# Kernel optimization log

Hardware: AMD Instinct MI355X
Metric: run time of the kernel (lower is better)

## Reference

```python
import jax, jax.numpy as jnp
import numpy as np

N0, N1, N2 = 100000, 25000, 6250
E0, E1, E2 = 600000, 150000, 37500
K = 6


def cheb_conv(x, edge_index, W, b):
    """torch_geometric ChebConv with sym normalization, lambda_max=2:
    L_hat = -D^{-1/2} A D^{-1/2}; T0=x, T1=L_hat x, Tk=2 L_hat T_{k-1} - T_{k-2}."""
    n = x.shape[0]
    src, dst = edge_index[0], edge_index[1]
    deg = jax.ops.segment_sum(jnp.ones(src.shape[0], x.dtype), src, num_segments=n)
    dinv = jnp.where(deg > 0, jax.lax.rsqrt(jnp.maximum(deg, 1.0)), 0.0)
    w = -(dinv[src] * dinv[dst])  # [E]

    def prop(h):  # (L_hat h)_i = sum_{j->i} w_ij h_j
        return jax.ops.segment_sum(w[:, None] * h[src], dst, num_segments=n)

    Tx0 = x
    out = Tx0 @ W[0]
    Tx1 = prop(x)
    out = out + Tx1 @ W[1]
    for k in range(2, W.shape[0]):
        Tx2 = 2.0 * prop(Tx1) - Tx0
        out = out + Tx2 @ W[k]
        Tx0, Tx1 = Tx1, Tx2
    return out + b


def pool(x, rows, cols, vals, n_out):
    # sparse.mm(D, x): y[r] += v * x[c]
    return jax.ops.segment_sum(vals[:, None] * x[cols], rows, num_segments=n_out)


def setup_inputs() -> dict:
    key = jax.random.key(0)
    ks = jax.random.split(key, 16)
    inp = {}
    inp["x"] = jax.random.normal(ks[0], (N0, 3), jnp.float32)
    inp["edge_index0"] = jax.random.randint(ks[1], (2, E0), 0, N0, jnp.int32)
    inp["edge_index1"] = jax.random.randint(ks[2], (2, E1), 0, N1, jnp.int32)
    inp["edge_index2"] = jax.random.randint(ks[3], (2, E2), 0, N2, jnp.int32)
    s = 0.05
    inp["W0"] = jax.random.normal(ks[4], (K, 3, 128), jnp.float32) * s
    inp["b0"] = jax.random.normal(ks[5], (128,), jnp.float32) * s
    inp["W1"] = jax.random.normal(ks[6], (K, 128, 128), jnp.float32) * s
    inp["b1"] = jax.random.normal(ks[7], (128,), jnp.float32) * s
    inp["W2"] = jax.random.normal(ks[8], (K, 128, 256), jnp.float32) * s
    inp["b2"] = jax.random.normal(ks[9], (256,), jnp.float32) * s
    inp["D0_rows"] = jax.random.randint(ks[10], (100000,), 0, N1, jnp.int32)
    inp["D0_cols"] = jax.random.randint(ks[11], (100000,), 0, N0, jnp.int32)
    inp["D0_vals"] = jax.random.uniform(ks[12], (100000,), jnp.float32)
    inp["D1_rows"] = jax.random.randint(ks[13], (25000,), 0, N2, jnp.int32)
    inp["D1_cols"] = jax.random.randint(ks[14], (25000,), 0, N1, jnp.int32)
    inp["D1_vals"] = jax.random.uniform(ks[15], (25000,), jnp.float32)
    k2 = jax.random.split(jax.random.fold_in(key, 1), 2)
    inp["linW"] = jax.random.normal(k2[0], (10, N2 * 256), jnp.float32) * 0.001
    inp["linb"] = jax.random.normal(k2[1], (10,), jnp.float32) * s
    return inp


def reference(x, edge_index0, edge_index1, edge_index2, W0, b0, W1, b1, W2, b2,
              D0_rows, D0_cols, D0_vals, D1_rows, D1_cols, D1_vals, linW, linb):
    h = jax.nn.relu(cheb_conv(x, edge_index0, W0, b0))      # [N0,128]
    h = pool(h, D0_rows, D0_cols, D0_vals, N1)               # [N1,128]
    h = jax.nn.relu(cheb_conv(h, edge_index1, W1, b1))      # [N1,128]
    h = pool(h, D1_rows, D1_cols, D1_vals, N2)               # [N2,128]
    h = cheb_conv(h, edge_index2, W2, b2)                    # [N2,256]
    Z = linW @ h.reshape(-1) + linb                           # [10]
    return Z
```

## Files before the change

kernel.cpp:

```cpp
#include <hip/hip_runtime.h>


namespace {
constexpr int cN0 = 100000, cN1 = 25000, cN2 = 6250;
constexpr int cE0 = 600000, cE1 = 150000, cE2 = 37500;
constexpr int cD  = cN2 * 256;

constexpr int JN[5]  = {cN0, cN1, cN2, cN1, cN2};
constexpr int JE[5]  = {cE0, cE1, cE2, 100000, 25000};
constexpr int JB[5]  = {391, 98, 25, 98, 25};
constexpr int JBBASE[6] = {0, 391, 489, 514, 612, 637};
constexpr int TB = 637;
constexpr int JCB[5] = {293, 74, 19, 49, 13};
constexpr int JCBASE[6] = {0, 293, 367, 386, 435, 448};
constexpr int TCB = 448;
constexpr int CHUNK = 2048;
constexpr int BSTRIDE = 400;

constexpr int EBASE[5]   = {0, 600000, 750000, 787500, 887500};
constexpr int E_TOTAL    = 912500;
constexpr int NBASE[5]   = {0, 100096, 125184, 131584, 156672};
constexpr int NPAD_TOTAL = 163072;
constexpr int DEGBASE[3] = {0, 100000, 125000};
constexpr int DEG_TOTAL  = 131250;
constexpr int WPREP_TOTAL = 768 * 128 + 768 * 256 + 128 * 32;
constexpr int PREP_ALL_TOTAL = WPREP_TOTAL + DEG_TOTAL + cN0 + 10;
}

typedef __attribute__((ext_vector_type(8))) short short8;
typedef __attribute__((ext_vector_type(4))) float floatx4;

__device__ inline ushort f2h(float f) {
  union { _Float16 h; ushort u; } v;
  v.h = (_Float16)f;
  return v.u;
}
__device__ inline float h2f(unsigned lo16) {
  union { ushort u; _Float16 h; } v;
  v.u = (ushort)lo16;
  return (float)v.h;
}

__device__ inline int job_of_cb(int cb) {
  int j = 0;
  while (cb >= JCBASE[j + 1]) ++j;
  return j;
}
__device__ inline int job_of_bucket(int g) {
  int j = 0;
  while (g >= JBBASE[j + 1]) ++j;
  return j;
}

__global__ __launch_bounds__(256) void c1_count_kernel(
    const int* __restrict__ k0, const int* __restrict__ k1, const int* __restrict__ k2,
    const int* __restrict__ k3, const int* __restrict__ k4,
    const int* __restrict__ s0, const int* __restrict__ s1, const int* __restrict__ s2,
    int* __restrict__ degcnt, int* __restrict__ cntCB) {
  __shared__ int cnt[BSTRIDE];
  int cb = blockIdx.x;
  int j = job_of_cb(cb);
  int lb = cb - JCBASE[j];
  const int* keys;
  const int* srck = nullptr;
  int dbase = 0;
  switch (j) {
    case 0: keys = k0; srck = s0; dbase = DEGBASE[0]; break;
    case 1: keys = k1; srck = s1; dbase = DEGBASE[1]; break;
    case 2: keys = k2; srck = s2; dbase = DEGBASE[2]; break;
    case 3: keys = k3; break;
    default: keys = k4; break;
  }
  int nB = JB[j];
  for (int b = threadIdx.x; b < nB; b += 256) cnt[b] = 0;
  __syncthreads();
  int e0 = lb * CHUNK;
  int e1 = min(e0 + CHUNK, JE[j]);
  for (int e = e0 + threadIdx.x; e < e1; e += 256) {
    atomicAdd(&cnt[keys[e] >> 8], 1);
    if (srck) atomicAdd(&degcnt[dbase + srck[e]], 1);
  }
  __syncthreads();
  for (int b = threadIdx.x; b < nB; b += 256)
    cntCB[cb * BSTRIDE + b] = cnt[b];
}

__global__ __launch_bounds__(256) void c2a_scan_kernel(int* __restrict__ cntCB,
                                                       int* __restrict__ bucketTot,
                                                       const int* __restrict__ degcnt,
                                                       float* __restrict__ dinv) {
  __shared__ int s[256];
  int g = blockIdx.x;
  int j = job_of_bucket(g);
  int b = g - JBBASE[j];
  int cb0 = JCBASE[j], nCB = JCB[j];
  int carry = 0;
  for (int c0 = 0; c0 < nCB; c0 += 256) {
    int i = c0 + threadIdx.x;
    int v = (i < nCB) ? cntCB[(cb0 + i) * BSTRIDE + b] : 0;
    s[threadIdx.x] = v;
    __syncthreads();
    for (int d = 1; d < 256; d <<= 1) {
      int t = (threadIdx.x >= d) ? s[threadIdx.x - d] : 0;
      __syncthreads();
      s[threadIdx.x] += t;
      __syncthreads();
    }
    if (i < nCB) cntCB[(cb0 + i) * BSTRIDE + b] = carry + s[threadIdx.x] - v;
    carry += s[255];
    __syncthreads();
  }
  if (threadIdx.x == 0) bucketTot[g] = carry;
  int idx = blockIdx.x * 256 + threadIdx.x;
  if (idx < DEG_TOTAL) {
    int c = degcnt[idx];
    dinv[idx] = (c > 0) ? rsqrtf((float)c) : 0.f;
  }
}

__global__ __launch_bounds__(256) void c2b_scan_kernel(const int* __restrict__ bucketTot,
                                                       int* __restrict__ bucketBase) {
  __shared__ int s[256];
  int j = blockIdx.x;
  int g0 = JBBASE[j], nB = JB[j];
  int carry = 0;
  for (int c0 = 0; c0 < nB; c0 += 256) {
    int i = c0 + threadIdx.x;
    int v = (i < nB) ? bucketTot[g0 + i] : 0;
    s[threadIdx.x] = v;
    __syncthreads();
    for (int d = 1; d < 256; d <<= 1) {
      int t = (threadIdx.x >= d) ? s[threadIdx.x - d] : 0;
      __syncthreads();
      s[threadIdx.x] += t;
      __syncthreads();
    }
    if (i < nB) bucketBase[g0 + i] = carry + s[threadIdx.x] - v;
    carry += s[255];
    __syncthreads();
  }
}

__global__ __launch_bounds__(256) void c3_dst_kernel(
    const int* __restrict__ d0, const int* __restrict__ s0,
    const int* __restrict__ d1, const int* __restrict__ s1,
    const int* __restrict__ d2, const int* __restrict__ s2,
    const int* __restrict__ p0r, const int* __restrict__ p0c, const float* __restrict__ p0v,
    const int* __restrict__ p1r, const int* __restrict__ p1c, const float* __restrict__ p1v,
    const float* __restrict__ dinv,
    const int* __restrict__ cntCB, const int* __restrict__ bucketBase,
    int2* __restrict__ scatPairs) {
  __shared__ int base[BSTRIDE];
  int cb = blockIdx.x;
  int j = job_of_cb(cb);
  int lb = cb - JCBASE[j];
  const int* dk; const int* sk; const float* vv = nullptr;
  switch (j) {
    case 0: dk = d0; sk = s0; break;
    case 1: dk = d1; sk = s1; break;
    case 2: dk = d2; sk = s2; break;
    case 3: dk = p0r; sk = p0c; vv = p0v; break;
    default: dk = p1r; sk = p1c; vv = p1v; break;
  }
  int nB = JB[j];
  for (int b = threadIdx.x; b < nB; b += 256)
    base[b] = EBASE[j] + bucketBase[JBBASE[j] + b] + cntCB[cb * BSTRIDE + b];
  __syncthreads();
  int e0 = lb * CHUNK;
  int e1 = min(e0 + CHUNK, JE[j]);
  for (int e = e0 + threadIdx.x; e < e1; e += 256) {
    int d = dk[e];
    int s = sk[e];
    float w;
    if (j < 3) w = -(dinv[DEGBASE[j] + s] * dinv[DEGBASE[j] + d]);
    else w = vv[e];
    int pos = atomicAdd(&base[d >> 8], 1);
    scatPairs[pos] = make_int2(((d & 255) << 17) | s, __float_as_int(w));
  }
}

__global__ __launch_bounds__(256) void dcsr_kernel(const int2* __restrict__ scatPairs,
                                                   const int* __restrict__ bucketTot,
                                                   const int* __restrict__ bucketBase,
                                                   int* __restrict__ off,
                                                   int2* __restrict__ csrPairs) {
  __shared__ int cnt[256];
  __shared__ int sArr[256];
  __shared__ int cur[256];
  int g = blockIdx.x;
  int j = job_of_bucket(g);
  int b = g - JBBASE[j];
  int relBase = bucketBase[g];
  int st = EBASE[j] + relBase;
  int en = st + bucketTot[g];
  cnt[threadIdx.x] = 0;
  __syncthreads();
  for (int idx = st + threadIdx.x; idx < en; idx += 256)
    atomicAdd(&cnt[scatPairs[idx].x >> 17], 1);
  __syncthreads();
  int v = cnt[threadIdx.x];
  sArr[threadIdx.x] = v;
  __syncthreads();
  for (int d = 1; d < 256; d <<= 1) {
    int t = (threadIdx.x >= d) ? sArr[threadIdx.x - d] : 0;
    __syncthreads();
    sArr[threadIdx.x] += t;
    __syncthreads();
  }
  int excl = sArr[threadIdx.x] - v;
  int node = b * 256 + threadIdx.x;
  if (node < JN[j]) off[NBASE[j] + node] = relBase + excl;
  if (threadIdx.x == 0 && b == JB[j] - 1) off[NBASE[j] + JN[j]] = JE[j];
  cur[threadIdx.x] = st + excl;
  __syncthreads();
  for (int idx = st + threadIdx.x; idx < en; idx += 256) {
    int2 p = scatPairs[idx];
    int dl = p.x >> 17;
    int s = p.x & 0x1FFFF;
    int pos = atomicAdd(&cur[dl], 1);
    csrPairs[pos] = make_int2(s, p.y);
  }
}

__global__ __launch_bounds__(256) void csr_prop128h_kernel(
    const int* __restrict__ off, const int2* __restrict__ pairs,
    const ushort* __restrict__ hh, float* __restrict__ y, ushort* __restrict__ yh,
    const float* __restrict__ prev, float scale, int N) {
  int r = blockIdx.x * 16 + (threadIdx.x >> 4);
  int l = threadIdx.x & 15;
  if (r >= N) return;
  int s = off[r], e = off[r + 1];
  const uint4* h4 = (const uint4*)hh;
  float a0 = 0.f, a1 = 0.f, a2 = 0.f, a3 = 0.f;
  float a4 = 0.f, a5 = 0.f, a6 = 0.f, a7 = 0.f;
  int j = s;
  for (; j + 4 <= e; j += 4) {
    int2 p0 = pairs[j], p1 = pairs[j + 1], p2 = pairs[j + 2], p3 = pairs[j + 3];
    uint4 v0 = h4[(size_t)p0.x * 16 + l];
    uint4 v1 = h4[(size_t)p1.x * 16 + l];
    uint4 v2 = h4[(size_t)p2.x * 16 + l];
    uint4 v3 = h4[(size_t)p3.x * 16 + l];
    float w0 = __int_as_float(p0.y), w1 = __int_as_float(p1.y);
    float w2 = __int_as_float(p2.y), w3 = __int_as_float(p3.y);
    a0 += w0 * h2f(v0.x & 0xFFFFu) + w1 * h2f(v1.x & 0xFFFFu)
        + w2 * h2f(v2.x & 0xFFFFu) + w3 * h2f(v3.x & 0xFFFFu);
    a1 += w0 * h2f(v0.x >> 16) + w1 * h2f(v1.x >> 16)
        + w2 * h2f(v2.x >> 16) + w3 * h2f(v3.x >> 16);
    a2 += w0 * h2f(v0.y & 0xFFFFu) + w1 * h2f(v1.y & 0xFFFFu)
        + w2 * h2f(v2.y & 0xFFFFu) + w3 * h2f(v3.y & 0xFFFFu);
    a3 += w0 * h2f(v0.y >> 16) + w1 * h2f(v1.y >> 16)
        + w2 * h2f(v2.y >> 16) + w3 * h2f(v3.y >> 16);
    a4 += w0 * h2f(v0.z & 0xFFFFu) + w1 * h2f(v1.z & 0xFFFFu)
        + w2 * h2f(v2.z & 0xFFFFu) + w3 * h2f(v3.z & 0xFFFFu);
    a5 += w0 * h2f(v0.z >> 16) + w1 * h2f(v1.z >> 16)
        + w2 * h2f(v2.z >> 16) + w3 * h2f(v3.z >> 16);
    a6 += w0 * h2f(v0.w & 0xFFFFu) + w1 * h2f(v1.w & 0xFFFFu)
        + w2 * h2f(v2.w & 0xFFFFu) + w3 * h2f(v3.w & 0xFFFFu);
    a7 += w0 * h2f(v0.w >> 16) + w1 * h2f(v1.w >> 16)
        + w2 * h2f(v2.w >> 16) + w3 * h2f(v3.w >> 16);
  }
  for (; j < e; ++j) {
    int2 p = pairs[j];
    uint4 v0 = h4[(size_t)p.x * 16 + l];
    float w = __int_as_float(p.y);
    a0 += w * h2f(v0.x & 0xFFFFu);
    a1 += w * h2f(v0.x >> 16);
    a2 += w * h2f(v0.y & 0xFFFFu);
    a3 += w * h2f(v0.y >> 16);
    a4 += w * h2f(v0.z & 0xFFFFu);
    a5 += w * h2f(v0.z >> 16);
    a6 += w * h2f(v0.w & 0xFFFFu);
    a7 += w * h2f(v0.w >> 16);
  }
  a0 *= scale; a1 *= scale; a2 *= scale; a3 *= scale;
  a4 *= scale; a5 *= scale; a6 *= scale; a7 *= scale;
  if (prev) {
    const float4* p4 = (const float4*)prev;
    float4 pa = p4[(size_t)r * 32 + 2 * l];
    float4 pb = p4[(size_t)r * 32 + 2 * l + 1];
    a0 -= pa.x; a1 -= pa.y; a2 -= pa.z; a3 -= pa.w;
    a4 -= pb.x; a5 -= pb.y; a6 -= pb.z; a7 -= pb.w;
  }
  if (y) {
    float4* y4 = (float4*)y;
    y4[(size_t)r * 32 + 2 * l]     = make_float4(a0, a1, a2, a3);
    y4[(size_t)r * 32 + 2 * l + 1] = make_float4(a4, a5, a6, a7);
  }
  uint4 sp;
  sp.x = f2h(a0) | ((unsigned)f2h(a1) << 16);
  sp.y = f2h(a2) | ((unsigned)f2h(a3) << 16);
  sp.z = f2h(a4) | ((unsigned)f2h(a5) << 16);
  sp.w = f2h(a6) | ((unsigned)f2h(a7) << 16);
  ((uint4*)yh)[(size_t)r * 16 + l] = sp;
}

__global__ __launch_bounds__(256) void csr_prop3_kernel(
    const int* __restrict__ off, const int2* __restrict__ pairs,
    const float4* __restrict__ h, float4* __restrict__ y,
    const float4* __restrict__ prev, float scale, int N,
    ushort* __restrict__ yh, int kout) {
  int t = blockIdx.x * 256 + threadIdx.x;
  int r = t >> 2;
  int q = t & 3;
  if (r >= N) return;
  int s = off[r], e = off[r + 1];
  float ax = 0.f, ay = 0.f, az = 0.f;
  for (int j = s + q; j < e; j += 4) {
    int2 p = pairs[j];
    float4 hv = h[p.x];
    float w = __int_as_float(p.y);
    ax += w * hv.x; ay += w * hv.y; az += w * hv.z;
  }
  ax += __shfl_xor(ax, 1); ay += __shfl_xor(ay, 1); az += __shfl_xor(az, 1);
  ax += __shfl_xor(ax, 2); ay += __shfl_xor(ay, 2); az += __shfl_xor(az, 2);
  if (q == 0) {
    float4 v = make_float4(scale * ax, scale * ay, scale * az, 0.f);
    if (prev) {
      float4 pv = prev[r];
      v.x -= pv.x; v.y -= pv.y; v.z -= pv.z;
    }
    y[r] = v;
    uint2 sp = make_uint2(f2h(v.x) | ((unsigned)f2h(v.y) << 16), (unsigned)f2h(v.z));
    *(uint2*)(yh + (size_t)r * 32 + kout * 4) = sp;
  }
}

__global__ __launch_bounds__(256, 2) void h0_mfma_kernel(
    const ushort* __restrict__ Ah, const ushort* __restrict__ W0h,
    const float* __restrict__ b0, ushort* __restrict__ h0h, int M) {
  __shared__ ushort Al[64][40];
  __shared__ ushort Bl[128][40];
  __shared__ ushort Hs[64][128];
  const int tid = threadIdx.x;
  const int rowBase = blockIdx.x * 64;
  const int wave = tid >> 6;
  const int lane = tid & 63;
  const int m16 = lane & 15;
  const int quad = lane >> 4;
  {
    int sRow = tid >> 2;
    int sK8 = (tid & 3) * 8;
    int row = rowBase + sRow;
    uint4 av = make_uint4(0, 0, 0, 0);
    if (row < M) av = *(const uint4*)(Ah + (size_t)row * 32 + sK8);
    *(uint4*)&Al[sRow][sK8] = av;
  }
#pragma unroll
  for (int l = 0; l < 2; ++l) {
    int lin = tid + l * 256;
    int bRow = lin >> 2;
    int bK8 = (lin & 3) * 8;
    *(uint4*)&Bl[bRow][bK8] = *(const uint4*)(W0h + (size_t)bRow * 32 + bK8);
  }
  __syncthreads();
  short8 a = *(const short8*)&Al[wave * 16 + m16][quad * 8];
  floatx4 acc[8];
#pragma unroll
  for (int c = 0; c < 8; ++c) {
    floatx4 z;
    z[0] = 0.f; z[1] = 0.f; z[2] = 0.f; z[3] = 0.f;
    short8 b = *(const short8*)&Bl[c * 16 + m16][quad * 8];
    acc[c] = __builtin_amdgcn_mfma_f32_16x16x32_f16(a, b, z, 0, 0, 0);
  }
#pragma unroll
  for (int c = 0; c < 8; ++c) {
    int col = c * 16 + m16;
    float bv = b0[col];
#pragma unroll
    for (int r = 0; r < 4; ++r)
      Hs[wave * 16 + quad * 4 + r][col] = f2h(fmaxf(acc[c][r] + bv, 0.f));
  }
  __syncthreads();
  const uint4* ls = (const uint4*)&Hs[0][0];
  uint4* gd = (uint4*)(h0h + (size_t)rowBase * 128);
#pragma unroll
  for (int i = 0; i < 4; ++i) {
    int idx = tid + i * 256;
    if (rowBase + (idx >> 4) < M) gd[idx] = ls[idx];
  }
}

__global__ void prep_all_kernel(const float* __restrict__ W0, const float* __restrict__ W1,
                                const float* __restrict__ W2, ushort* __restrict__ W0h,
                                ushort* __restrict__ Wt1, ushort* __restrict__ Wt2,
                                int* __restrict__ degcnt,
                                const float* __restrict__ x, float4* __restrict__ Tb,
                                ushort* __restrict__ Ah,
                                float* __restrict__ out, const float* __restrict__ linb) {
  int i = blockIdx.x * 256 + threadIdx.x;
  if (i < 768 * 128) {
    int k = i / 128, n = i - k * 128;
    Wt1[(size_t)n * 768 + k] = f2h(W1[i]);
  } else if (i < 768 * 128 + 768 * 256) {
    int i2 = i - 768 * 128;
    int k = i2 / 256, n = i2 - k * 256;
    Wt2[(size_t)n * 768 + k] = f2h(W2[i2]);
  } else if (i < WPREP_TOTAL) {
    int i3 = i - 768 * 128 - 768 * 256;
    int col = i3 >> 5, k = i3 & 31;
    int a = k >> 2, jj = k & 3;
    float v = (k < 24 && jj < 3) ? W0[(a * 3 + jj) * 128 + col] : 0.f;
    W0h[(size_t)col * 32 + k] = f2h(v);
  } else if (i < WPREP_TOTAL + DEG_TOTAL) {
    degcnt[i - WPREP_TOTAL] = 0;
  } else if (i < WPREP_TOTAL + DEG_TOTAL + cN0) {
    int r = i - (WPREP_TOTAL + DEG_TOTAL);
    float x0 = x[3 * r], x1 = x[3 * r + 1], x2 = x[3 * r + 2];
    Tb[r] = make_float4(x0, x1, x2, 0.f);
    uint4 z = make_uint4(0, 0, 0, 0);
    uint4 first = make_uint4(f2h(x0) | ((unsigned)f2h(x1) << 16), (unsigned)f2h(x2), 0, 0);
    uint4* p = (uint4*)(Ah + (size_t)r * 32);
    p[0] = first; p[1] = z; p[2] = z; p[3] = z;
  } else if (i < PREP_ALL_TOTAL) {
    int o = i - (WPREP_TOTAL + DEG_TOTAL + cN0);
    out[o] = linb[o];
  }
}

template <int RELU, int OUTH>
__global__ __launch_bounds__(256, 2) void gemm_mfma_kernel(
    const ushort* __restrict__ Th, const ushort* __restrict__ Wt,
    const float* __restrict__ bias, float* __restrict__ C, ushort* __restrict__ Ch,
    int M, int N) {
  __shared__ ushort Al[64][40];
  __shared__ ushort Bl[128][40];
  __shared__ ushort Hs[64][128];
  const int tid = threadIdx.x;
  const int rowBase = blockIdx.x * 64;
  const int colBase = blockIdx.y * 128;
  const int wave = tid >> 6;
  const int lane = tid & 63;
  const int m16 = lane & 15;
  const int quad = lane >> 4;
  const size_t Mstride = (size_t)M * 128;

  floatx4 acc[8];
#pragma unroll
  for (int c = 0; c < 8; ++c)
#pragma unroll
    for (int r = 0; r < 4; ++r) acc[c][r] = 0.f;

  const int sRow = tid >> 2;
  const int sK8 = (tid & 3) * 8;
  const int growA = rowBase + sRow;
  const bool aValid = growA < M;

  for (int kc = 0; kc < 24; ++kc) {
    uint4 av = make_uint4(0, 0, 0, 0);
    if (aValid)
      av = *(const uint4*)(Th + (size_t)(kc >> 2) * Mstride + (size_t)growA * 128
                           + ((kc & 3) << 5) + sK8);
    *(uint4*)&Al[sRow][sK8] = av;
#pragma unroll
    for (int l = 0; l < 2; ++l) {
      int lin = tid + l * 256;
      int bRow = lin >> 2;
      int bK8 = (lin & 3) * 8;
      *(uint4*)&Bl[bRow][bK8] =
          *(const uint4*)(Wt + (size_t)(colBase + bRow) * 768 + kc * 32 + bK8);
    }
    __syncthreads();

    short8 a = *(const short8*)&Al[wave * 16 + m16][quad * 8];
#pragma unroll
    for (int c = 0; c < 8; ++c) {
      short8 b = *(const short8*)&Bl[c * 16 + m16][quad * 8];
      acc[c] = __builtin_amdgcn_mfma_f32_16x16x32_f16(a, b, acc[c], 0, 0, 0);
    }
    __syncthreads();
  }

  if (OUTH) {
#pragma unroll
    for (int c = 0; c < 8; ++c) {
      int col = c * 16 + m16;
      float bv = bias[col];
#pragma unroll
      for (int r = 0; r < 4; ++r) {
        float v = acc[c][r] + bv;
        if (RELU) v = fmaxf(v, 0.f);
        Hs[wave * 16 + quad * 4 + r][col] = f2h(v);
      }
    }
    __syncthreads();
    const uint4* ls = (const uint4*)&Hs[0][0];
    uint4* gd = (uint4*)(Ch + (size_t)rowBase * 128);
#pragma unroll
    for (int i = 0; i < 4; ++i) {
      int idx = tid + i * 256;
      if (rowBase + (idx >> 4) < M) gd[idx] = ls[idx];
    }
  } else {
#pragma unroll
    for (int c = 0; c < 8; ++c) {
      int col = colBase + c * 16 + m16;
      float bv = bias[col];
#pragma unroll
      for (int r = 0; r < 4; ++r) {
        int row = rowBase + wave * 16 + quad * 4 + r;
        if (row < M) {
          float v = acc[c][r] + bv;
          if (RELU) v = fmaxf(v, 0.f);
          C[(size_t)row * N + col] = v;
        }
      }
    }
  }
}

__global__ __launch_bounds__(256) void linear_kernel(const float* __restrict__ Wl,
                                                     const float* __restrict__ h,
                                                     float* __restrict__ out, int D) {
  float p[10];
#pragma unroll
  for (int j = 0; j < 10; ++j) p[j] = 0.f;
  int stride = gridDim.x * blockDim.x;
  for (int i = blockIdx.x * blockDim.x + threadIdx.x; i < D; i += stride) {
    float hv = h[i];
#pragma unroll
    for (int j = 0; j < 10; ++j) p[j] += Wl[(size_t)j * D + i] * hv;
  }
#pragma unroll
  for (int j = 0; j < 10; ++j) {
#pragma unroll
    for (int off = 32; off > 0; off >>= 1) p[j] += __shfl_down(p[j], off, 64);
  }
  __shared__ float s[4][10];
  int wave = threadIdx.x >> 6, lane = threadIdx.x & 63;
  if (lane == 0) {
#pragma unroll
    for (int j = 0; j < 10; ++j) s[wave][j] = p[j];
  }
  __syncthreads();
  if (threadIdx.x < 10) {
    float t = s[0][threadIdx.x] + s[1][threadIdx.x] + s[2][threadIdx.x] + s[3][threadIdx.x];
    atomicAdd(&out[threadIdx.x], t);
  }
}

extern "C" void kernel_launch(void* const* d_in, const int* in_sizes, int n_in,
                              void* d_out, int out_size, void* d_ws, size_t ws_size,
                              hipStream_t stream) {
  const float* x    = (const float*)d_in[0];
  const int*   ei0  = (const int*)d_in[1];
  const int*   ei1  = (const int*)d_in[2];
  const int*   ei2  = (const int*)d_in[3];
  const float* W0   = (const float*)d_in[4];
  const float* b0   = (const float*)d_in[5];
  const float* W1   = (const float*)d_in[6];
  const float* b1   = (const float*)d_in[7];
  const float* W2   = (const float*)d_in[8];
  const float* b2   = (const float*)d_in[9];
  const int*   D0r  = (const int*)d_in[10];
  const int*   D0c  = (const int*)d_in[11];
  const float* D0v  = (const float*)d_in[12];
  const int*   D1r  = (const int*)d_in[13];
  const int*   D1c  = (const int*)d_in[14];
  const float* D1v  = (const float*)d_in[15];
  const float* linW = (const float*)d_in[16];
  const float* linb = (const float*)d_in[17];
  float* out = (float*)d_out;
  (void)in_sizes; (void)n_in; (void)out_size; (void)ws_size;

  const int* src0 = ei0;            const int* dst0 = ei0 + cE0;
  const int* src1 = ei1;            const int* dst1 = ei1 + cE1;
  const int* src2 = ei2;            const int* dst2 = ei2 + cE2;

  float* ws = (float*)d_ws;
  size_t off = 0;
  auto alloc = [&](size_t n) {
    float* p = ws + off;
    off += (n + 63) & ~size_t(63);
    return p;
  };
  float* dinv       = alloc(DEG_TOTAL);
  int*   degcnt     = (int*)alloc(DEG_TOTAL);
  int*   cntCB      = (int*)alloc((size_t)TCB * BSTRIDE);
  int*   bucketTot  = (int*)alloc(TB);
  int*   bucketBase = (int*)alloc(TB);
  int2*  scatPairs  = (int2*)alloc((size_t)2 * E_TOTAL);
  int2*  csrPairs   = (int2*)alloc((size_t)2 * E_TOTAL);
  int*   offArr     = (int*)alloc(NPAD_TOTAL);
  ushort* W0h       = (ushort*)alloc(128 * 32 / 2);
  ushort* Wt1       = (ushort*)alloc(768 * 128 / 2);
  ushort* Wt2       = (ushort*)alloc(768 * 256 / 2);
  float4* Tb0       = (float4*)alloc((size_t)6 * cN0 * 4);
  ushort* Ah0       = (ushort*)alloc((size_t)cN0 * 16);
  ushort* h0h       = (ushort*)alloc((size_t)cN0 * 64);
  float* Tlvl1      = alloc((size_t)6 * cN1 * 128);
  ushort* Th1       = (ushort*)alloc((size_t)6 * cN1 * 64);
  ushort* out1h     = (ushort*)alloc((size_t)cN1 * 64);
  float* Tlvl2      = alloc((size_t)6 * cN2 * 128);
  ushort* Th2       = (ushort*)alloc((size_t)6 * cN2 * 64);
  float* out2       = alloc((size_t)cN2 * 256);

  auto nb = [](long long n) { return (unsigned)((n + 255) / 256); };

  prep_all_kernel<<<nb(PREP_ALL_TOTAL), 256, 0, stream>>>(
      W0, W1, W2, W0h, Wt1, Wt2, degcnt, x, Tb0, Ah0, out, linb);

  c1_count_kernel<<<TCB, 256, 0, stream>>>(dst0, dst1, dst2, D0r, D1r,
                                           src0, src1, src2, degcnt, cntCB);
  c2a_scan_kernel<<<TB, 256, 0, stream>>>(cntCB, bucketTot, degcnt, dinv);
  c2b_scan_kernel<<<5, 256, 0, stream>>>(bucketTot, bucketBase);
  c3_dst_kernel<<<TCB, 256, 0, stream>>>(dst0, src0, dst1, src1, dst2, src2,
                                         D0r, D0c, D0v, D1r, D1c, D1v,
                                         dinv, cntCB, bucketBase, scatPairs);
  dcsr_kernel<<<TB, 256, 0, stream>>>(scatPairs, bucketTot, bucketBase,
                                      offArr, csrPairs);

  auto seg_off   = [&](int s) { return offArr + NBASE[s]; };
  auto seg_pairs = [&](int s) { return csrPairs + EBASE[s]; };

  {
    auto Tk = [&](int k) { return Tb0 + (size_t)k * cN0; };
    csr_prop3_kernel<<<nb((size_t)4 * cN0), 256, 0, stream>>>(seg_off(0), seg_pairs(0),
        Tk(0), Tk(1), nullptr, 1.f, cN0, Ah0, 1);
    csr_prop3_kernel<<<nb((size_t)4 * cN0), 256, 0, stream>>>(seg_off(0), seg_pairs(0),
        Tk(1), Tk(2), Tk(0), 2.f, cN0, Ah0, 2);
    csr_prop3_kernel<<<nb((size_t)4 * cN0), 256, 0, stream>>>(seg_off(0), seg_pairs(0),
        Tk(2), Tk(3), Tk(1), 2.f, cN0, Ah0, 3);
    csr_prop3_kernel<<<nb((size_t)4 * cN0), 256, 0, stream>>>(seg_off(0), seg_pairs(0),
        Tk(3), Tk(4), Tk(2), 2.f, cN0, Ah0, 4);
    csr_prop3_kernel<<<nb((size_t)4 * cN0), 256, 0, stream>>>(seg_off(0), seg_pairs(0),
        Tk(4), Tk(5), Tk(3), 2.f, cN0, Ah0, 5);
  }
  h0_mfma_kernel<<<(cN0 + 63) / 64, 256, 0, stream>>>(Ah0, W0h, b0, h0h, cN0);
  csr_prop128h_kernel<<<(cN1 + 15) / 16, 256, 0, stream>>>(
      seg_off(3), seg_pairs(3), h0h, Tlvl1, Th1, nullptr, 1.f, cN1);

  {
    auto Tk  = [&](int k) { return Tlvl1 + (size_t)k * cN1 * 128; };
    auto Thk = [&](int k) { return Th1 + (size_t)k * cN1 * 128; };
    auto prop = [&](int kin, int kout, int kprev, float scale, bool needF32) {
      csr_prop128h_kernel<<<(cN1 + 15) / 16, 256, 0, stream>>>(
          seg_off(1), seg_pairs(1), Thk(kin), needF32 ? Tk(kout) : nullptr, Thk(kout),
          (kprev >= 0) ? Tk(kprev) : nullptr, scale, cN1);
    };
    prop(0, 1, -1, 1.f, true);
    prop(1, 2, 0, 2.f, true);
    prop(2, 3, 1, 2.f, true);
    prop(3, 4, 2, 2.f, true);
    prop(4, 5, 3, 2.f, false);
    dim3 g((cN1 + 63) / 64, 1);
    gemm_mfma_kernel<1, 1><<<g, 256, 0, stream>>>(Th1, Wt1, b1, nullptr, out1h,
                                                  cN1, 128);
  }

  csr_prop128h_kernel<<<(cN2 + 15) / 16, 256, 0, stream>>>(
      seg_off(4), seg_pairs(4), out1h, Tlvl2, Th2, nullptr, 1.f, cN2);

  {
    auto Tk  = [&](int k) { return Tlvl2 + (size_t)k * cN2 * 128; };
    auto Thk = [&](int k) { return Th2 + (size_t)k * cN2 * 128; };
    auto prop = [&](int kin, int kout, int kprev, float scale, bool needF32) {
      csr_prop128h_kernel<<<(cN2 + 15) / 16, 256, 0, stream>>>(
          seg_off(2), seg_pairs(2), Thk(kin), needF32 ? Tk(kout) : nullptr, Thk(kout),
          (kprev >= 0) ? Tk(kprev) : nullptr, scale, cN2);
    };
    prop(0, 1, -1, 1.f, true);
    prop(1, 2, 0, 2.f, true);
    prop(2, 3, 1, 2.f, true);
    prop(3, 4, 2, 2.f, true);
    prop(4, 5, 3, 2.f, false);
    dim3 g((cN2 + 63) / 64, 2);
    gemm_mfma_kernel<0, 0><<<g, 256, 0, stream>>>(Th2, Wt2, b2, out2, nullptr,
                                                  cN2, 256);
  }

  linear_kernel<<<512, 256, 0, stream>>>(linW, out2, out, cD);
}
```

Baseline: 410.9 us.

## Drop fp32 level-1 Chebyshev buffers and precompute per-node CSR offsets in count pass

Measured after the change: 434.1 us. 5.6% more time.

```diff
diff --git a/kernel.cpp b/kernel.cpp
--- a/kernel.cpp
+++ b/kernel.cpp
@@ -24,7 +24,7 @@
 constexpr int DEGBASE[3] = {0, 100000, 125000};
 constexpr int DEG_TOTAL  = 131250;
 constexpr int WPREP_TOTAL = 768 * 128 + 768 * 256 + 128 * 32;
-constexpr int PREP_ALL_TOTAL = WPREP_TOTAL + DEG_TOTAL + cN0 + 10;
+constexpr int PREP_ALL_TOTAL = WPREP_TOTAL + DEG_TOTAL + NPAD_TOTAL + cN0 + 10;
 }
 
 typedef __attribute__((ext_vector_type(8))) short short8;
@@ -56,7 +56,7 @@
     const int* __restrict__ k0, const int* __restrict__ k1, const int* __restrict__ k2,
     const int* __restrict__ k3, const int* __restrict__ k4,
     const int* __restrict__ s0, const int* __restrict__ s1, const int* __restrict__ s2,
-    int* __restrict__ degcnt, int* __restrict__ cntCB) {
+    int* __restrict__ degcnt, int* __restrict__ nodecnt, int* __restrict__ cntCB) {
   __shared__ int cnt[BSTRIDE];
   int cb = blockIdx.x;
   int j = job_of_cb(cb);
@@ -72,12 +72,15 @@
     default: keys = k4; break;
   }
   int nB = JB[j];
+  int nb = NBASE[j];
   for (int b = threadIdx.x; b < nB; b += 256) cnt[b] = 0;
   __syncthreads();
   int e0 = lb * CHUNK;
   int e1 = min(e0 + CHUNK, JE[j]);
   for (int e = e0 + threadIdx.x; e < e1; e += 256) {
-    atomicAdd(&cnt[keys[e] >> 8], 1);
+    int d = keys[e];
+    atomicAdd(&cnt[d >> 8], 1);
+    atomicAdd(&nodecnt[nb + d], 1);
     if (srck) atomicAdd(&degcnt[dbase + srck[e]], 1);
   }
   __syncthreads();
@@ -139,6 +142,26 @@
     carry += s[255];
     __syncthreads();
   }
+}
+
+__global__ __launch_bounds__(256) void nodescan_kernel(
+    const int* __restrict__ nodecnt, const int* __restrict__ bucketBase,
+    int* __restrict__ offArr) {
+  __shared__ int s[256];
+  int g = blockIdx.x;
+  int j = job_of_bucket(g);
+  int b = g - JBBASE[j];
+  int idx = NBASE[j] + b * 256 + threadIdx.x;
+  int v = nodecnt[idx];
+  s[threadIdx.x] = v;
+  __syncthreads();
+  for (int d = 1; d < 256; d <<= 1) {
+    int t = (threadIdx.x >= d) ? s[threadIdx.x - d] : 0;
+    __syncthreads();
+    s[threadIdx.x] += t;
+    __syncthreads();
+  }
+  offArr[idx] = bucketBase[g] + s[threadIdx.x] - v;
 }
 
 __global__ __launch_bounds__(256) void c3_dst_kernel(
@@ -179,39 +202,17 @@
   }
 }
 
-__global__ __launch_bounds__(256) void dcsr_kernel(const int2* __restrict__ scatPairs,
-                                                   const int* __restrict__ bucketTot,
-                                                   const int* __restrict__ bucketBase,
-                                                   int* __restrict__ off,
-                                                   int2* __restrict__ csrPairs) {
-  __shared__ int cnt[256];
-  __shared__ int sArr[256];
+__global__ __launch_bounds__(256) void dcsr2_kernel(
+    const int2* __restrict__ scatPairs, const int* __restrict__ bucketTot,
+    const int* __restrict__ bucketBase, const int* __restrict__ offArr,
+    int2* __restrict__ csrPairs) {
   __shared__ int cur[256];
   int g = blockIdx.x;
   int j = job_of_bucket(g);
   int b = g - JBBASE[j];
-  int relBase = bucketBase[g];
-  int st = EBASE[j] + relBase;
+  int st = EBASE[j] + bucketBase[g];
   int en = st + bucketTot[g];
-  cnt[threadIdx.x] = 0;
-  __syncthreads();
-  for (int idx = st + threadIdx.x; idx < en; idx += 256)
-    atomicAdd(&cnt[scatPairs[idx].x >> 17], 1);
-  __syncthreads();
-  int v = cnt[threadIdx.x];
-  sArr[threadIdx.x] = v;
-  __syncthreads();
-  for (int d = 1; d < 256; d <<= 1) {
-    int t = (threadIdx.x >= d) ? sArr[threadIdx.x - d] : 0;
-    __syncthreads();
-    sArr[threadIdx.x] += t;
-    __syncthreads();
-  }
-  int excl = sArr[threadIdx.x] - v;
-  int node = b * 256 + threadIdx.x;
-  if (node < JN[j]) off[NBASE[j] + node] = relBase + excl;
-  if (threadIdx.x == 0 && b == JB[j] - 1) off[NBASE[j] + JN[j]] = JE[j];
-  cur[threadIdx.x] = st + excl;
+  cur[threadIdx.x] = EBASE[j] + offArr[NBASE[j] + b * 256 + threadIdx.x];
   __syncthreads();
   for (int idx = st + threadIdx.x; idx < en; idx += 256) {
     int2 p = scatPairs[idx];
@@ -225,7 +226,8 @@
 __global__ __launch_bounds__(256) void csr_prop128h_kernel(
     const int* __restrict__ off, const int2* __restrict__ pairs,
     const ushort* __restrict__ hh, float* __restrict__ y, ushort* __restrict__ yh,
-    const float* __restrict__ prev, float scale, int N) {
+    const float* __restrict__ prevF, const ushort* __restrict__ prevH,
+    float scale, int N) {
   int r = blockIdx.x * 16 + (threadIdx.x >> 4);
   int l = threadIdx.x & 15;
   if (r >= N) return;
@@ -274,12 +276,18 @@
   }
   a0 *= scale; a1 *= scale; a2 *= scale; a3 *= scale;
   a4 *= scale; a5 *= scale; a6 *= scale; a7 *= scale;
-  if (prev) {
-    const float4* p4 = (const float4*)prev;
+  if (prevF) {
+    const float4* p4 = (const float4*)prevF;
     float4 pa = p4[(size_t)r * 32 + 2 * l];
     float4 pb = p4[(size_t)r * 32 + 2 * l + 1];
     a0 -= pa.x; a1 -= pa.y; a2 -= pa.z; a3 -= pa.w;
     a4 -= pb.x; a5 -= pb.y; a6 -= pb.z; a7 -= pb.w;
+  } else if (prevH) {
+    uint4 pv = ((const uint4*)prevH)[(size_t)r * 16 + l];
+    a0 -= h2f(pv.x & 0xFFFFu); a1 -= h2f(pv.x >> 16);
+    a2 -= h2f(pv.y & 0xFFFFu); a3 -= h2f(pv.y >> 16);
+    a4 -= h2f(pv.z & 0xFFFFu); a5 -= h2f(pv.z >> 16);
+    a6 -= h2f(pv.w & 0xFFFFu); a7 -= h2f(pv.w >> 16);
   }
   if (y) {
     float4* y4 = (float4*)y;
@@ -383,7 +391,7 @@
 __global__ void prep_all_kernel(const float* __restrict__ W0, const float* __restrict__ W1,
                                 const float* __restrict__ W2, ushort* __restrict__ W0h,
                                 ushort* __restrict__ Wt1, ushort* __restrict__ Wt2,
-                                int* __restrict__ degcnt,
+                                int* __restrict__ degcnt, int* __restrict__ nodecnt,
                                 const float* __restrict__ x, float4* __restrict__ Tb,
                                 ushort* __restrict__ Ah,
                                 float* __restrict__ out, const float* __restrict__ linb) {
@@ -403,8 +411,10 @@
     W0h[(size_t)col * 32 + k] = f2h(v);
   } else if (i < WPREP_TOTAL + DEG_TOTAL) {
     degcnt[i - WPREP_TOTAL] = 0;
-  } else if (i < WPREP_TOTAL + DEG_TOTAL + cN0) {
-    int r = i - (WPREP_TOTAL + DEG_TOTAL);
+  } else if (i < WPREP_TOTAL + DEG_TOTAL + NPAD_TOTAL) {
+    nodecnt[i - (WPREP_TOTAL + DEG_TOTAL)] = 0;
+  } else if (i < WPREP_TOTAL + DEG_TOTAL + NPAD_TOTAL + cN0) {
+    int r = i - (WPREP_TOTAL + DEG_TOTAL + NPAD_TOTAL);
     float x0 = x[3 * r], x1 = x[3 * r + 1], x2 = x[3 * r + 2];
     Tb[r] = make_float4(x0, x1, x2, 0.f);
     uint4 z = make_uint4(0, 0, 0, 0);
@@ -412,7 +422,7 @@
     uint4* p = (uint4*)(Ah + (size_t)r * 32);
     p[0] = first; p[1] = z; p[2] = z; p[3] = z;
   } else if (i < PREP_ALL_TOTAL) {
-    int o = i - (WPREP_TOTAL + DEG_TOTAL + cN0);
+    int o = i - (WPREP_TOTAL + DEG_TOTAL + NPAD_TOTAL + cN0);
     out[o] = linb[o];
   }
 }
@@ -575,6 +585,7 @@
   };
   float* dinv       = alloc(DEG_TOTAL);
   int*   degcnt     = (int*)alloc(DEG_TOTAL);
+  int*   nodecnt    = (int*)alloc(NPAD_TOTAL);
   int*   cntCB      = (int*)alloc((size_t)TCB * BSTRIDE);
   int*   bucketTot  = (int*)alloc(TB);
   int*   bucketBase = (int*)alloc(TB);
@@ -587,7 +598,6 @@
   float4* Tb0       = (float4*)alloc((size_t)6 * cN0 * 4);
   ushort* Ah0       = (ushort*)alloc((size_t)cN0 * 16);
   ushort* h0h       = (ushort*)alloc((size_t)cN0 * 64);
-  float* Tlvl1      = alloc((size_t)6 * cN1 * 128);
   ushort* Th1       = (ushort*)alloc((size_t)6 * cN1 * 64);
   ushort* out1h     = (ushort*)alloc((size_t)cN1 * 64);
   float* Tlvl2      = alloc((size_t)6 * cN2 * 128);
@@ -597,17 +607,18 @@
   auto nb = [](long long n) { return (unsigned)((n + 255) / 256); };
 
   prep_all_kernel<<<nb(PREP_ALL_TOTAL), 256, 0, stream>>>(
-      W0, W1, W2, W0h, Wt1, Wt2, degcnt, x, Tb0, Ah0, out, linb);
+      W0, W1, W2, W0h, Wt1, Wt2, degcnt, nodecnt, x, Tb0, Ah0, out, linb);
 
   c1_count_kernel<<<TCB, 256, 0, stream>>>(dst0, dst1, dst2, D0r, D1r,
-                                           src0, src1, src2, degcnt, cntCB);
+                                           src0, src1, src2, degcnt, nodecnt, cntCB);
   c2a_scan_kernel<<<TB, 256, 0, stream>>>(cntCB, bucketTot, degcnt, dinv);
   c2b_scan_kernel<<<5, 256, 0, stream>>>(bucketTot, bucketBase);
+  nodescan_kernel<<<TB, 256, 0, stream>>>(nodecnt, bucketBase, offArr);
   c3_dst_kernel<<<TCB, 256, 0, stream>>>(dst0, src0, dst1, src1, dst2, src2,
                                          D0r, D0c, D0v, D1r, D1c, D1v,
                                          dinv, cntCB, bucketBase, scatPairs);
-  dcsr_kernel<<<TB, 256, 0, stream>>>(scatPairs, bucketTot, bucketBase,
-                                      offArr, csrPairs);
+  dcsr2_kernel<<<TB, 256, 0, stream>>>(scatPairs, bucketTot, bucketBase,
+                                       offArr, csrPairs);
 
   auto seg_off   = [&](int s) { return offArr + NBASE[s]; };
   auto seg_pairs = [&](int s) { return csrPairs + EBASE[s]; };
@@ -627,28 +638,27 @@
   }
   h0_mfma_kernel<<<(cN0 + 63) / 64, 256, 0, stream>>>(Ah0, W0h, b0, h0h, cN0);
   csr_prop128h_kernel<<<(cN1 + 15) / 16, 256, 0, stream>>>(
-      seg_off(3), seg_pairs(3), h0h, Tlvl1, Th1, nullptr, 1.f, cN1);
+      seg_off(3), seg_pairs(3), h0h, nullptr, Th1, nullptr, nullptr, 1.f, cN1);
 
   {
-    auto Tk  = [&](int k) { return Tlvl1 + (size_t)k * cN1 * 128; };
     auto Thk = [&](int k) { return Th1 + (size_t)k * cN1 * 128; };
-    auto prop = [&](int kin, int kout, int kprev, float scale, bool needF32) {
+    auto prop = [&](int kin, int kout, int kprev, float scale) {
       csr_prop128h_kernel<<<(cN1 + 15) / 16, 256, 0, stream>>>(
-          seg_off(1), seg_pairs(1), Thk(kin), needF32 ? Tk(kout) : nullptr, Thk(kout),
-          (kprev >= 0) ? Tk(kprev) : nullptr, scale, cN1);
+          seg_off(1), seg_pairs(1), Thk(kin), nullptr, Thk(kout),
+          nullptr, (kprev >= 0) ? Thk(kprev) : nullptr, scale, cN1);
     };
-    prop(0, 1, -1, 1.f, true);
-    prop(1, 2, 0, 2.f, true);
-    prop(2, 3, 1, 2.f, true);
-    prop(3, 4, 2, 2.f, true);
-    prop(4, 5, 3, 2.f, false);
+    prop(0, 1, -1, 1.f);
+    prop(1, 2, 0, 2.f);
+    prop(2, 3, 1, 2.f);
+    prop(3, 4, 2, 2.f);
+    prop(4, 5, 3, 2.f);
     dim3 g((cN1 + 63) / 64, 1);
     gemm_mfma_kernel<1, 1><<<g, 256, 0, stream>>>(Th1, Wt1, b1, nullptr, out1h,
                                                   cN1, 128);
   }
 
   csr_prop128h_kernel<<<(cN2 + 15) / 16, 256, 0, stream>>>(
-      seg_off(4), seg_pairs(4), out1h, Tlvl2, Th2, nullptr, 1.f, cN2);
+      seg_off(4), seg_pairs(4), out1h, Tlvl2, Th2, nullptr, nullptr, 1.f, cN2);
 
   {
     auto Tk  = [&](int k) { return Tlvl2 + (size_t)k * cN2 * 128; };
@@ -656,7 +666,7 @@
     auto prop = [&](int kin, int kout, int kprev, float scale, bool needF32) {
       csr_prop128h_kernel<<<(cN2 + 15) / 16, 256, 0, stream>>>(
           seg_off(2), seg_pairs(2), Thk(kin), needF32 ? Tk(kout) : nullptr, Thk(kout),
-          (kprev >= 0) ? Tk(kprev) : nullptr, scale, cN2);
+          (kprev >= 0) ? Tk(kprev) : nullptr, nullptr, scale, cN2);
     };
     prop(0, 1, -1, 1.f, true);
     prop(1, 2, 0, 2.f, true);
```
